# Kernel tuning notes

Measured on AMD Instinct MI355X. Metric: run time of the kernel, lower is better.

The kernel has to match this reference:

```python
import jax, jax.numpy as jnp
import numpy as np

N, E, F, H, O = 50000, 800000, 64, 128, 64
GRID_SIZE, SPLINE_ORDER = 3, 2


def make_grid(in_features, grid_size=GRID_SIZE, spline_order=SPLINE_ORDER, grid_range=(-1.0, 1.0)):
    h = (grid_range[1] - grid_range[0]) / grid_size
    pts = jnp.arange(-spline_order, grid_size + spline_order + 1, dtype=jnp.float32) * h + grid_range[0]
    return jnp.tile(pts[None, :], (in_features, 1))  # [in, grid_size + 2*order + 1]


def b_splines(x, grid, spline_order=SPLINE_ORDER):
    # x: [B, in], grid: [in, G+2k+1] -> bases [B, in, G+k]
    xe = x[..., None]
    bases = ((xe >= grid[:, :-1]) & (xe < grid[:, 1:])).astype(x.dtype)
    for k in range(1, spline_order + 1):
        bases = ((xe - grid[:, : -(k + 1)]) / (grid[:, k:-1] - grid[:, : -(k + 1)]) * bases[..., :-1]
                 + (grid[:, k + 1:] - xe) / (grid[:, k + 1:] - grid[:, 1:-k]) * bases[..., 1:])
    return bases


def setup_inputs() -> dict:
    key = jax.random.key(0)
    ks = jax.random.split(key, 12)
    x = jax.random.normal(ks[0], (N, F), dtype=jnp.float32)
    contexts = jax.random.normal(ks[1], (E, F), dtype=jnp.float32)
    attn = jax.random.uniform(ks[2], (E,), dtype=jnp.float32)
    seg_ids = jnp.sort(jax.random.randint(ks[3], (E,), 0, N, dtype=jnp.int32))
    s = 0.05
    Wn = jax.random.normal(ks[4], (H, F), dtype=jnp.float32) * s
    bn = jnp.zeros((H,), dtype=jnp.float32)
    Wc = jax.random.normal(ks[5], (H, F), dtype=jnp.float32) * s
    bc = jnp.zeros((H,), dtype=jnp.float32)
    Wu = jax.random.normal(ks[6], (O, H), dtype=jnp.float32) * s
    bu = jnp.zeros((O,), dtype=jnp.float32)
    n_coef = GRID_SIZE + SPLINE_ORDER
    base_w = jax.random.normal(ks[7], (O, O), dtype=jnp.float32) * s
    spline_w = jax.random.normal(ks[8], (O, O, n_coef), dtype=jnp.float32) * s
    spline_scaler = jnp.ones((O, O), dtype=jnp.float32)
    grid = make_grid(O)
    return dict(x=x, contexts=contexts, attn=attn, seg_ids=seg_ids, Wn=Wn, bn=bn,
                Wc=Wc, bc=bc, Wu=Wu, bu=bu, base_w=base_w, spline_w=spline_w,
                spline_scaler=spline_scaler, grid=grid)


def reference(x, contexts, attn, seg_ids, Wn, bn, Wc, bc, Wu, bu, base_w, spline_w, spline_scaler, grid):
    n = x.shape[0]
    # per-edge context transform, attention weighting
    ctx_t = contexts @ Wc.T + bc                      # [E, H]
    weighted = ctx_t * attn[:, None]                  # [E, H]
    seg_sum = jax.ops.segment_sum(weighted, seg_ids, num_segments=n)        # [N, H]
    deg = jax.ops.segment_sum(jnp.ones_like(attn), seg_ids, num_segments=n)  # [N]
    ctx_agg = seg_sum / jnp.maximum(deg, 1.0)[:, None]  # mean over edges per node
    x_t = x @ Wn.T + bn                               # [N, H]
    upd = (x_t + ctx_agg) @ Wu.T + bu                 # [N, O]
    # KANLinear (efficient-kan): silu base path + b-spline path
    base_out = jax.nn.silu(upd) @ base_w.T            # [N, O]
    bases = b_splines(upd, grid)                      # [N, O, G+k]
    scaled_sw = spline_w * spline_scaler[..., None]   # [O, O, G+k]
    spline_out = jnp.einsum('bik,oik->bo', bases, scaled_sw)
    kan_out = base_out + spline_out
    # nodes with no contexts keep their raw features (num_features == output_dim)
    return jnp.where(deg[:, None] > 0, kan_out, x)
```

## Files before the change

### kernel.cpp

```cpp
#include <hip/hip_runtime.h>
#include <hip/hip_bf16.h>

#define NN 50000
#define NE 800000

typedef short short8 __attribute__((ext_vector_type(8)));
typedef float f32x4 __attribute__((ext_vector_type(4)));
typedef unsigned short ushort_t;

static __device__ __forceinline__ unsigned bits(float f) { return __float_as_uint(f); }
static __device__ __forceinline__ float hi_f(float v) {
  return __uint_as_float(bits(v) & 0xFFFF0000u);
}
static __device__ __forceinline__ ushort_t hi_u(float v) { return (ushort_t)(bits(v) >> 16); }
static __device__ __forceinline__ unsigned pack_hi(float v0, float v1) {
  return (bits(v0) >> 16) | (bits(v1) & 0xFFFF0000u);
}
static __device__ __forceinline__ unsigned pack_lo(float v0, float v1) {
  float l0 = v0 - hi_f(v0), l1 = v1 - hi_f(v1);
  return (bits(l0) >> 16) | (bits(l1) & 0xFFFF0000u);
}

#define MFMA(a, b, c) __builtin_amdgcn_mfma_f32_16x16x32_bf16(a, b, c, 0, 0, 0)

__global__ __launch_bounds__(256) void kA_pack_off(
    const float* __restrict__ Wn, const float* __restrict__ Wc,
    const float* __restrict__ Wu, const float* __restrict__ base_w,
    const float* __restrict__ spline_w, const float* __restrict__ scaler,
    const int* __restrict__ seg,
    ushort_t* __restrict__ p1h, ushort_t* __restrict__ p2h,
    ushort_t* __restrict__ p3h, int* __restrict__ off) {
  int t = blockIdx.x * 256 + threadIdx.x;
  if (t < 4096) {
    int l = t & 63, lm = l & 15, lk = l >> 4;
    if (t < 2048) {
      int nt = t >> 8, ks = (t >> 6) & 3;
      int h = nt * 16 + lm;
#pragma unroll
      for (int j = 0; j < 8; ++j) {
        int f = ks * 32 + lk * 8 + j;
        float v = (f < 64) ? Wn[h * 64 + f] : Wc[h * 64 + (f - 64)];
        p1h[t * 8 + j] = hi_u(v);
      }
    }
    if (t < 1024) {
      int nt = t >> 8, ks = (t >> 6) & 3;
      int o = nt * 16 + lm;
#pragma unroll
      for (int j = 0; j < 8; ++j) {
        int hh = ks * 32 + lk * 8 + j;
        p2h[t * 8 + j] = hi_u(Wu[o * 128 + hh]);
      }
    }
    if (t < 3072) {
      int nt = t / 768, ks = (t >> 6) % 12;
      int o = nt * 16 + lm;
#pragma unroll
      for (int j = 0; j < 8; ++j) {
        int k = ks * 32 + lk * 8 + j;
        int i = k / 6, c = k % 6;
        float v = (c == 0) ? base_w[o * 64 + i]
                           : spline_w[(o * 64 + i) * 5 + (c - 1)] * scaler[o * 64 + i];
        p3h[t * 8 + j] = hi_u(v);
      }
    }
  }
  int e = t;
  if (e < NE) {
    int s1 = seg[e];
    if (e == 0) {
      for (int n = 0; n <= s1; ++n) off[n] = 0;
    } else {
      int s0 = seg[e - 1];
      for (int n = s0 + 1; n <= s1; ++n) off[n] = e;
    }
    if (e == NE - 1) {
      for (int n = s1 + 1; n <= NN; ++n) off[n] = NE;
    }
  }
}

__global__ __launch_bounds__(256) void k1_edge_agg(
    const float* __restrict__ contexts, const float* __restrict__ attn,
    const int* __restrict__ off, ushort_t* __restrict__ Sph,
    ushort_t* __restrict__ Spl, float* __restrict__ aprime,
    float* __restrict__ degw) {
  int n = blockIdx.x * 4 + (threadIdx.x >> 6);
  int lane = threadIdx.x & 63;
  if (n >= NN) return;
  int s = off[n];
  int e_end = off[n + 1];
  int deg_i = e_end - s;

  int sub = lane >> 4;
  int fq = lane & 15;
  const float4* ctx4 = (const float4*)contexts;

  float4 S = make_float4(0.f, 0.f, 0.f, 0.f);
  float A = 0.f;
  if (deg_i > 0) {
    int last = e_end - 1;
    for (int e0 = s; e0 < e_end; e0 += 16) {
      float a[4];
      float4 c[4];
#pragma unroll
      for (int u = 0; u < 4; ++u) {
        int eu = e0 + 4 * u + sub;
        a[u] = (eu < e_end) ? attn[eu] : 0.f;
        c[u] = ctx4[(size_t)min(eu, last) * 16 + fq];
      }
#pragma unroll
      for (int u = 0; u < 4; ++u) {
        S.x += a[u] * c[u].x;
        S.y += a[u] * c[u].y;
        S.z += a[u] * c[u].z;
        S.w += a[u] * c[u].w;
        A += a[u];
      }
    }
  }
#pragma unroll
  for (int m = 16; m <= 32; m <<= 1) {
    S.x += __shfl_xor(S.x, m);
    S.y += __shfl_xor(S.y, m);
    S.z += __shfl_xor(S.z, m);
    S.w += __shfl_xor(S.w, m);
    A += __shfl_xor(A, m);
  }
  float deg = (float)deg_i;
  float inv = 1.f / fmaxf(deg, 1.f);
  if (lane < 16) {
    float ox = S.x * inv, oy = S.y * inv, oz = S.z * inv, ow = S.w * inv;
    uint2 hp, lp;
    hp.x = pack_hi(ox, oy);
    hp.y = pack_hi(oz, ow);
    lp.x = pack_lo(ox, oy);
    lp.y = pack_lo(oz, ow);
    *(uint2*)&Sph[(size_t)n * 64 + lane * 4] = hp;
    *(uint2*)&Spl[(size_t)n * 64 + lane * 4] = lp;
  }
  if (lane == 0) { aprime[n] = A * inv; degw[n] = deg; }
}

__global__ __launch_bounds__(256, 3) void k234(
    const float* __restrict__ x,
    const ushort_t* __restrict__ Sph, const ushort_t* __restrict__ Spl,
    const float* __restrict__ aprime, const float* __restrict__ degw,
    const float* __restrict__ bn, const float* __restrict__ bc,
    const float* __restrict__ bu,
    const ushort_t* __restrict__ p1h, const ushort_t* __restrict__ p2h,
    const ushort_t* __restrict__ p3h,
    const float* __restrict__ gridp, float* __restrict__ out) {
  __shared__ __align__(16) unsigned char arena[49152];
  __shared__ float ap[64], degl[64];
  ushort_t* Uh = (ushort_t*)arena;
  ushort_t* Ul = (ushort_t*)(arena + 16384);
  ushort_t* Th = (ushort_t*)(arena + 32768);
  ushort_t* Vh = (ushort_t*)arena;

  int tid = threadIdx.x;
  int n0 = blockIdx.x * 64;
  int w = tid >> 6, l = tid & 63;
  int lm = l & 15, lk = l >> 4;
  const short8* P1h = (const short8*)p1h;
  const short8* P2h = (const short8*)p2h;
  const short8* P3h = (const short8*)p3h;

  short8 B1[2][4], B2[4];
#pragma unroll
  for (int q2 = 0; q2 < 2; ++q2)
#pragma unroll
    for (int ks = 0; ks < 4; ++ks) B1[q2][ks] = P1h[((2 * w + q2) * 4 + ks) * 64 + l];
#pragma unroll
  for (int ks = 0; ks < 4; ++ks) B2[ks] = P2h[(w * 4 + ks) * 64 + l];

  float g[8];
#pragma unroll
  for (int j = 0; j < 8; ++j) g[j] = gridp[j];
  float r1[7], r2[6];
#pragma unroll
  for (int j = 0; j < 7; ++j) r1[j] = 1.f / (g[j + 1] - g[j]);
#pragma unroll
  for (int j = 0; j < 6; ++j) r2[j] = 1.f / (g[j + 2] - g[j]);
  float buv = bu[w * 16 + lm];

  {
    const float4* x4 = (const float4*)x;
    const uint4* Sh4 = (const uint4*)Sph;
    const uint4* Sl4 = (const uint4*)Spl;
    for (int q = tid; q < 1024; q += 256) {
      int row = q >> 4, slot = q & 15;
      int n = n0 + row;
      int idx = (row * 128 + slot * 8) ^ ((row & 7) << 3);
      if (slot < 8) {
        float4 a = make_float4(0.f, 0.f, 0.f, 0.f), b = a;
        if (n < NN) {
          a = x4[(size_t)n * 16 + slot * 2];
          b = x4[(size_t)n * 16 + slot * 2 + 1];
        }
        uint4 hp, lp;
        hp.x = pack_hi(a.x, a.y); hp.y = pack_hi(a.z, a.w);
        hp.z = pack_hi(b.x, b.y); hp.w = pack_hi(b.z, b.w);
        lp.x = pack_lo(a.x, a.y); lp.y = pack_lo(a.z, a.w);
        lp.z = pack_lo(b.x, b.y); lp.w = pack_lo(b.z, b.w);
        *(uint4*)&Uh[idx] = hp;
        *(uint4*)&Ul[idx] = lp;
      } else {
        uint4 vh = make_uint4(0u, 0u, 0u, 0u), vl = vh;
        if (n < NN) {
          vh = Sh4[(size_t)n * 8 + (slot & 7)];
          vl = Sl4[(size_t)n * 8 + (slot & 7)];
        }
        *(uint4*)&Uh[idx] = vh;
        *(uint4*)&Ul[idx] = vl;
      }
    }
  }
  if (tid < 64) {
    int n = n0 + tid;
    ap[tid] = (n < NN) ? aprime[n] : 0.f;
    degl[tid] = (n < NN) ? degw[n] : 1.f;
  }
  __syncthreads();

  int swzA = (lm & 7) << 3;

  f32x4 acc1[2][4];
#pragma unroll
  for (int q2 = 0; q2 < 2; ++q2)
#pragma unroll
    for (int mt = 0; mt < 4; ++mt) acc1[q2][mt] = (f32x4){0.f, 0.f, 0.f, 0.f};
#pragma unroll
  for (int ks = 0; ks < 4; ++ks) {
    short8 ah[4], al[4];
#pragma unroll
    for (int mt = 0; mt < 4; ++mt) {
      int ai = ((mt * 16 + lm) * 128 + ks * 32 + lk * 8) ^ swzA;
      ah[mt] = *(const short8*)&Uh[ai];
      al[mt] = *(const short8*)&Ul[ai];
    }
#pragma unroll
    for (int q2 = 0; q2 < 2; ++q2)
#pragma unroll
      for (int mt = 0; mt < 4; ++mt) {
        acc1[q2][mt] = MFMA(ah[mt], B1[q2][ks], acc1[q2][mt]);
        acc1[q2][mt] = MFMA(al[mt], B1[q2][ks], acc1[q2][mt]);
      }
  }
#pragma unroll
  for (int q2 = 0; q2 < 2; ++q2) {
    int h = (2 * w + q2) * 16 + lm;
    float bnv = bn[h], bcv = bc[h];
#pragma unroll
    for (int mt = 0; mt < 4; ++mt) {
#pragma unroll
      for (int r = 0; r < 4; ++r) {
        int node = mt * 16 + lk * 4 + r;
        float t = acc1[q2][mt][r] + bnv + ap[node] * bcv;
        Th[(node * 128 + h) ^ ((node & 7) << 3)] = hi_u(t);
      }
    }
  }
  __syncthreads();

  short8 B3[12];
#pragma unroll
  for (int ks = 0; ks < 12; ++ks) B3[ks] = P3h[(w * 12 + ks) * 64 + l];

  f32x4 acc2[4];
#pragma unroll
  for (int mt = 0; mt < 4; ++mt) acc2[mt] = (f32x4){0.f, 0.f, 0.f, 0.f};
#pragma unroll
  for (int ks = 0; ks < 4; ++ks) {
#pragma unroll
    for (int mt = 0; mt < 4; ++mt) {
      int ai = ((mt * 16 + lm) * 128 + ks * 32 + lk * 8) ^ swzA;
      short8 ah = *(const short8*)&Th[ai];
      acc2[mt] = MFMA(ah, B2[ks], acc2[mt]);
    }
  }

#pragma unroll
  for (int half = 0; half < 2; ++half) {
#pragma unroll
    for (int ms = 0; ms < 2; ++ms) {
      int mt = half * 2 + ms;
#pragma unroll
      for (int r = 0; r < 4; ++r) {
        float xv = acc2[mt][r] + buv;
        float sil = xv / (1.f + __expf(-xv));
        float b0[7], b1[6], b2[5];
#pragma unroll
        for (int q = 0; q < 7; ++q) b0[q] = (xv >= g[q] && xv < g[q + 1]) ? 1.f : 0.f;
#pragma unroll
        for (int q = 0; q < 6; ++q)
          b1[q] = (xv - g[q]) * r1[q] * b0[q] + (g[q + 2] - xv) * r1[q + 1] * b0[q + 1];
#pragma unroll
        for (int q = 0; q < 5; ++q)
          b2[q] = (xv - g[q]) * r2[q] * b1[q] + (g[q + 3] - xv) * r2[q + 1] * b1[q + 1];
        int ln = ms * 16 + lk * 4 + r;
        int base = ln * 392 + (w * 16 + lm) * 6;
        *(unsigned*)&Vh[base + 0] = pack_hi(sil, b2[0]);
        *(unsigned*)&Vh[base + 2] = pack_hi(b2[1], b2[2]);
        *(unsigned*)&Vh[base + 4] = pack_hi(b2[3], b2[4]);
      }
    }
    __syncthreads();

    f32x4 accK[2];
    accK[0] = (f32x4){0.f, 0.f, 0.f, 0.f};
    accK[1] = (f32x4){0.f, 0.f, 0.f, 0.f};
#pragma unroll
    for (int ks = 0; ks < 12; ++ks) {
#pragma unroll
      for (int s = 0; s < 2; ++s) {
        short8 ah = *(const short8*)&Vh[(s * 16 + lm) * 392 + ks * 32 + lk * 8];
        accK[s] = MFMA(ah, B3[ks], accK[s]);
      }
    }
    if (half == 0) __syncthreads();

#pragma unroll
    for (int s = 0; s < 2; ++s) {
      int o = w * 16 + lm;
#pragma unroll
      for (int r = 0; r < 4; ++r) {
        int node = half * 32 + s * 16 + lk * 4 + r;
        int n = n0 + node;
        if (n < NN) {
          float val = accK[s][r];
          if (degl[node] <= 0.f) val = x[(size_t)n * 64 + o];
          out[(size_t)n * 64 + o] = val;
        }
      }
    }
  }
}

extern "C" void kernel_launch(void* const* d_in, const int* in_sizes, int n_in,
                              void* d_out, int out_size, void* d_ws, size_t ws_size,
                              hipStream_t stream) {
  const float* x        = (const float*)d_in[0];
  const float* contexts = (const float*)d_in[1];
  const float* attn     = (const float*)d_in[2];
  const int*   seg      = (const int*)d_in[3];
  const float* Wn       = (const float*)d_in[4];
  const float* bn       = (const float*)d_in[5];
  const float* Wc       = (const float*)d_in[6];
  const float* bc       = (const float*)d_in[7];
  const float* Wu       = (const float*)d_in[8];
  const float* bu       = (const float*)d_in[9];
  const float* base_w   = (const float*)d_in[10];
  const float* spline_w = (const float*)d_in[11];
  const float* scaler   = (const float*)d_in[12];
  const float* gridp    = (const float*)d_in[13];
  float* out = (float*)d_out;

  ushort_t* us  = (ushort_t*)d_ws;
  ushort_t* Sph = us;
  ushort_t* Spl = Sph + 3200000;
  ushort_t* p1h = Spl + 3200000;
  ushort_t* p2h = p1h + 16384;
  ushort_t* p3h = p2h + 8192;
  float* aprime = (float*)(p3h + 24576);
  float* degw   = aprime + 50000;
  int*   off    = (int*)(degw + 50000);

  kA_pack_off<<<3125, 256, 0, stream>>>(Wn, Wc, Wu, base_w, spline_w, scaler, seg,
                                        p1h, p2h, p3h, off);
  k1_edge_agg<<<12500, 256, 0, stream>>>(contexts, attn, off, Sph, Spl, aprime, degw);
  k234<<<782, 256, 0, stream>>>(x, Sph, Spl, aprime, degw, bn, bc, bu,
                                p1h, p2h, p3h, gridp, out);
}
```

Measured before the change: 73.15 us.

## Fuse edge aggregation into node MLP/KAN kernel with 512-thread blocks

Merges the per-node edge aggregation kernel into the dense node kernel, so each 64-node block first reduces its own edges straight into shared memory instead of writing and reading back split-bf16 aggregates, attn means and degrees through global memory. Blocks grow to 8 waves, split 2x4 over node and output tiles, and each wave aggregates 8 nodes serially. This removes one launch and the intermediate global traffic. In exchange only 782 blocks carry the whole edge gather, and the irregular, latency-bound gather now runs serially per wave in the same kernel as the MFMA stages, which may lower latency hiding.

```diff
diff --git a/kernel.cpp b/kernel.cpp
--- a/kernel.cpp
+++ b/kernel.cpp
@@ -80,72 +80,10 @@
   }
 }
 
-__global__ __launch_bounds__(256) void k1_edge_agg(
+__global__ __launch_bounds__(512, 4) void k1234(
+    const float* __restrict__ x,
     const float* __restrict__ contexts, const float* __restrict__ attn,
-    const int* __restrict__ off, ushort_t* __restrict__ Sph,
-    ushort_t* __restrict__ Spl, float* __restrict__ aprime,
-    float* __restrict__ degw) {
-  int n = blockIdx.x * 4 + (threadIdx.x >> 6);
-  int lane = threadIdx.x & 63;
-  if (n >= NN) return;
-  int s = off[n];
-  int e_end = off[n + 1];
-  int deg_i = e_end - s;
-
-  int sub = lane >> 4;
-  int fq = lane & 15;
-  const float4* ctx4 = (const float4*)contexts;
-
-  float4 S = make_float4(0.f, 0.f, 0.f, 0.f);
-  float A = 0.f;
-  if (deg_i > 0) {
-    int last = e_end - 1;
-    for (int e0 = s; e0 < e_end; e0 += 16) {
-      float a[4];
-      float4 c[4];
-#pragma unroll
-      for (int u = 0; u < 4; ++u) {
-        int eu = e0 + 4 * u + sub;
-        a[u] = (eu < e_end) ? attn[eu] : 0.f;
-        c[u] = ctx4[(size_t)min(eu, last) * 16 + fq];
-      }
-#pragma unroll
-      for (int u = 0; u < 4; ++u) {
-        S.x += a[u] * c[u].x;
-        S.y += a[u] * c[u].y;
-        S.z += a[u] * c[u].z;
-        S.w += a[u] * c[u].w;
-        A += a[u];
-      }
-    }
-  }
-#pragma unroll
-  for (int m = 16; m <= 32; m <<= 1) {
-    S.x += __shfl_xor(S.x, m);
-    S.y += __shfl_xor(S.y, m);
-    S.z += __shfl_xor(S.z, m);
-    S.w += __shfl_xor(S.w, m);
-    A += __shfl_xor(A, m);
-  }
-  float deg = (float)deg_i;
-  float inv = 1.f / fmaxf(deg, 1.f);
-  if (lane < 16) {
-    float ox = S.x * inv, oy = S.y * inv, oz = S.z * inv, ow = S.w * inv;
-    uint2 hp, lp;
-    hp.x = pack_hi(ox, oy);
-    hp.y = pack_hi(oz, ow);
-    lp.x = pack_lo(ox, oy);
-    lp.y = pack_lo(oz, ow);
-    *(uint2*)&Sph[(size_t)n * 64 + lane * 4] = hp;
-    *(uint2*)&Spl[(size_t)n * 64 + lane * 4] = lp;
-  }
-  if (lane == 0) { aprime[n] = A * inv; degw[n] = deg; }
-}
-
-__global__ __launch_bounds__(256, 3) void k234(
-    const float* __restrict__ x,
-    const ushort_t* __restrict__ Sph, const ushort_t* __restrict__ Spl,
-    const float* __restrict__ aprime, const float* __restrict__ degw,
+    const int* __restrict__ off,
     const float* __restrict__ bn, const float* __restrict__ bc,
     const float* __restrict__ bu,
     const ushort_t* __restrict__ p1h, const ushort_t* __restrict__ p2h,
@@ -161,19 +99,144 @@
   int tid = threadIdx.x;
   int n0 = blockIdx.x * 64;
   int w = tid >> 6, l = tid & 63;
+  int wm = w >> 2, wn = w & 3;
   int lm = l & 15, lk = l >> 4;
   const short8* P1h = (const short8*)p1h;
   const short8* P2h = (const short8*)p2h;
   const short8* P3h = (const short8*)p3h;
 
+  {
+    const float4* x4 = (const float4*)x;
+    int row = tid >> 3, slot = tid & 7;
+    int n = n0 + row;
+    float4 a = make_float4(0.f, 0.f, 0.f, 0.f), b = a;
+    if (n < NN) {
+      a = x4[(size_t)n * 16 + slot * 2];
+      b = x4[(size_t)n * 16 + slot * 2 + 1];
+    }
+    uint4 hp, lp;
+    hp.x = pack_hi(a.x, a.y); hp.y = pack_hi(a.z, a.w);
+    hp.z = pack_hi(b.x, b.y); hp.w = pack_hi(b.z, b.w);
+    lp.x = pack_lo(a.x, a.y); lp.y = pack_lo(a.z, a.w);
+    lp.z = pack_lo(b.x, b.y); lp.w = pack_lo(b.z, b.w);
+    int idx = (row * 128 + slot * 8) ^ ((row & 7) << 3);
+    *(uint4*)&Uh[idx] = hp;
+    *(uint4*)&Ul[idx] = lp;
+  }
+
+  {
+    int nb = n0 + w * 8;
+    int offv = 0;
+    if (l < 9) offv = off[min(nb + l, NN)];
+    int sub = l >> 4, fq = l & 15;
+    const float4* ctx4 = (const float4*)contexts;
+#pragma unroll 1
+    for (int i = 0; i < 8; ++i) {
+      int s = __shfl(offv, i);
+      int e_end = __shfl(offv, i + 1);
+      int deg_i = e_end - s;
+      float4 S = make_float4(0.f, 0.f, 0.f, 0.f);
+      float A = 0.f;
+      if (deg_i > 0) {
+        int last = e_end - 1;
+        for (int e0 = s; e0 < e_end; e0 += 16) {
+          float a[4];
+          float4 c[4];
+#pragma unroll
+          for (int u = 0; u < 4; ++u) {
+            int eu = e0 + 4 * u + sub;
+            a[u] = (eu < e_end) ? attn[eu] : 0.f;
+            c[u] = ctx4[(size_t)min(eu, last) * 16 + fq];
+          }
+#pragma unroll
+          for (int u = 0; u < 4; ++u) {
+            S.x += a[u] * c[u].x;
+            S.y += a[u] * c[u].y;
+            S.z += a[u] * c[u].z;
+            S.w += a[u] * c[u].w;
+            A += a[u];
+          }
+        }
+      }
+#pragma unroll
+      for (int m = 16; m <= 32; m <<= 1) {
+        S.x += __shfl_xor(S.x, m);
+        S.y += __shfl_xor(S.y, m);
+        S.z += __shfl_xor(S.z, m);
+        S.w += __shfl_xor(S.w, m);
+        A += __shfl_xor(A, m);
+      }
+      float deg = (float)deg_i;
+      float inv = 1.f / fmaxf(deg, 1.f);
+      int row = w * 8 + i;
+      if (l < 16) {
+        float ox = S.x * inv, oy = S.y * inv, oz = S.z * inv, ow = S.w * inv;
+        uint2 hp, lp;
+        hp.x = pack_hi(ox, oy);
+        hp.y = pack_hi(oz, ow);
+        lp.x = pack_lo(ox, oy);
+        lp.y = pack_lo(oz, ow);
+        int idx = (row * 128 + 64 + l * 4) ^ ((row & 7) << 3);
+        *(uint2*)&Uh[idx] = hp;
+        *(uint2*)&Ul[idx] = lp;
+      }
+      if (l == 0) { ap[row] = A * inv; degl[row] = deg; }
+    }
+  }
+
   short8 B1[2][4], B2[4];
 #pragma unroll
-  for (int q2 = 0; q2 < 2; ++q2)
-#pragma unroll
-    for (int ks = 0; ks < 4; ++ks) B1[q2][ks] = P1h[((2 * w + q2) * 4 + ks) * 64 + l];
-#pragma unroll
-  for (int ks = 0; ks < 4; ++ks) B2[ks] = P2h[(w * 4 + ks) * 64 + l];
-
+  for (int q = 0; q < 2; ++q)
+#pragma unroll
+    for (int ks = 0; ks < 4; ++ks) B1[q][ks] = P1h[((2 * wn + q) * 4 + ks) * 64 + l];
+#pragma unroll
+  for (int ks = 0; ks < 4; ++ks) B2[ks] = P2h[(wn * 4 + ks) * 64 + l];
+
+  __syncthreads();
+
+  int swzA = (lm & 7) << 3;
+
+  f32x4 acc1[2][2];
+#pragma unroll
+  for (int q = 0; q < 2; ++q)
+#pragma unroll
+    for (int ms = 0; ms < 2; ++ms) acc1[q][ms] = (f32x4){0.f, 0.f, 0.f, 0.f};
+#pragma unroll
+  for (int ks = 0; ks < 4; ++ks) {
+    short8 ah[2], al[2];
+#pragma unroll
+    for (int ms = 0; ms < 2; ++ms) {
+      int ai = (((2 * wm + ms) * 16 + lm) * 128 + ks * 32 + lk * 8) ^ swzA;
+      ah[ms] = *(const short8*)&Uh[ai];
+      al[ms] = *(const short8*)&Ul[ai];
+    }
+#pragma unroll
+    for (int q = 0; q < 2; ++q)
+#pragma unroll
+      for (int ms = 0; ms < 2; ++ms) {
+        acc1[q][ms] = MFMA(ah[ms], B1[q][ks], acc1[q][ms]);
+        acc1[q][ms] = MFMA(al[ms], B1[q][ks], acc1[q][ms]);
+      }
+  }
+#pragma unroll
+  for (int q = 0; q < 2; ++q) {
+    int h = (2 * wn + q) * 16 + lm;
+    float bnv = bn[h], bcv = bc[h];
+#pragma unroll
+    for (int ms = 0; ms < 2; ++ms) {
+#pragma unroll
+      for (int r = 0; r < 4; ++r) {
+        int node = (2 * wm + ms) * 16 + lk * 4 + r;
+        float t = acc1[q][ms][r] + bnv + ap[node] * bcv;
+        Th[(node * 128 + h) ^ ((node & 7) << 3)] = hi_u(t);
+      }
+    }
+  }
+  __syncthreads();
+
+  short8 B3[12];
+#pragma unroll
+  for (int ks = 0; ks < 12; ++ks) B3[ks] = P3h[(wn * 12 + ks) * 64 + l];
   float g[8];
 #pragma unroll
   for (int j = 0; j < 8; ++j) g[j] = gridp[j];
@@ -182,156 +245,66 @@
   for (int j = 0; j < 7; ++j) r1[j] = 1.f / (g[j + 1] - g[j]);
 #pragma unroll
   for (int j = 0; j < 6; ++j) r2[j] = 1.f / (g[j + 2] - g[j]);
-  float buv = bu[w * 16 + lm];
-
-  {
-    const float4* x4 = (const float4*)x;
-    const uint4* Sh4 = (const uint4*)Sph;
-    const uint4* Sl4 = (const uint4*)Spl;
-    for (int q = tid; q < 1024; q += 256) {
-      int row = q >> 4, slot = q & 15;
-      int n = n0 + row;
-      int idx = (row * 128 + slot * 8) ^ ((row & 7) << 3);
-      if (slot < 8) {
-        float4 a = make_float4(0.f, 0.f, 0.f, 0.f), b = a;
-        if (n < NN) {
-          a = x4[(size_t)n * 16 + slot * 2];
-          b = x4[(size_t)n * 16 + slot * 2 + 1];
+  float buv = bu[wn * 16 + lm];
+
+  f32x4 acc2[2];
+  acc2[0] = (f32x4){0.f, 0.f, 0.f, 0.f};
+  acc2[1] = (f32x4){0.f, 0.f, 0.f, 0.f};
+#pragma unroll
+  for (int ks = 0; ks < 4; ++ks) {
+#pragma unroll
+    for (int ms = 0; ms < 2; ++ms) {
+      int ai = (((2 * wm + ms) * 16 + lm) * 128 + ks * 32 + lk * 8) ^ swzA;
+      short8 ah = *(const short8*)&Th[ai];
+      acc2[ms] = MFMA(ah, B2[ks], acc2[ms]);
+    }
+  }
+
+#pragma unroll
+  for (int half = 0; half < 2; ++half) {
+    if (wm == half) {
+#pragma unroll
+      for (int ms = 0; ms < 2; ++ms) {
+#pragma unroll
+        for (int r = 0; r < 4; ++r) {
+          float xv = acc2[ms][r] + buv;
+          float sil = xv / (1.f + __expf(-xv));
+          float b0[7], b1[6], b2[5];
+#pragma unroll
+          for (int q = 0; q < 7; ++q) b0[q] = (xv >= g[q] && xv < g[q + 1]) ? 1.f : 0.f;
+#pragma unroll
+          for (int q = 0; q < 6; ++q)
+            b1[q] = (xv - g[q]) * r1[q] * b0[q] + (g[q + 2] - xv) * r1[q + 1] * b0[q + 1];
+#pragma unroll
+          for (int q = 0; q < 5; ++q)
+            b2[q] = (xv - g[q]) * r2[q] * b1[q] + (g[q + 3] - xv) * r2[q + 1] * b1[q + 1];
+          int ln = ms * 16 + lk * 4 + r;
+          int base = ln * 392 + (wn * 16 + lm) * 6;
+          *(unsigned*)&Vh[base + 0] = pack_hi(sil, b2[0]);
+          *(unsigned*)&Vh[base + 2] = pack_hi(b2[1], b2[2]);
+          *(unsigned*)&Vh[base + 4] = pack_hi(b2[3], b2[4]);
         }
-        uint4 hp, lp;
-        hp.x = pack_hi(a.x, a.y); hp.y = pack_hi(a.z, a.w);
-        hp.z = pack_hi(b.x, b.y); hp.w = pack_hi(b.z, b.w);
-        lp.x = pack_lo(a.x, a.y); lp.y = pack_lo(a.z, a.w);
-        lp.z = pack_lo(b.x, b.y); lp.w = pack_lo(b.z, b.w);
-        *(uint4*)&Uh[idx] = hp;
-        *(uint4*)&Ul[idx] = lp;
-      } else {
-        uint4 vh = make_uint4(0u, 0u, 0u, 0u), vl = vh;
-        if (n < NN) {
-          vh = Sh4[(size_t)n * 8 + (slot & 7)];
-          vl = Sl4[(size_t)n * 8 + (slot & 7)];
-        }
-        *(uint4*)&Uh[idx] = vh;
-        *(uint4*)&Ul[idx] = vl;
-      }
-    }
-  }
-  if (tid < 64) {
-    int n = n0 + tid;
-    ap[tid] = (n < NN) ? aprime[n] : 0.f;
-    degl[tid] = (n < NN) ? degw[n] : 1.f;
-  }
-  __syncthreads();
-
-  int swzA = (lm & 7) << 3;
-
-  f32x4 acc1[2][4];
-#pragma unroll
-  for (int q2 = 0; q2 < 2; ++q2)
-#pragma unroll
-    for (int mt = 0; mt < 4; ++mt) acc1[q2][mt] = (f32x4){0.f, 0.f, 0.f, 0.f};
-#pragma unroll
-  for (int ks = 0; ks < 4; ++ks) {
-    short8 ah[4], al[4];
-#pragma unroll
-    for (int mt = 0; mt < 4; ++mt) {
-      int ai = ((mt * 16 + lm) * 128 + ks * 32 + lk * 8) ^ swzA;
-      ah[mt] = *(const short8*)&Uh[ai];
-      al[mt] = *(const short8*)&Ul[ai];
-    }
-#pragma unroll
-    for (int q2 = 0; q2 < 2; ++q2)
-#pragma unroll
-      for (int mt = 0; mt < 4; ++mt) {
-        acc1[q2][mt] = MFMA(ah[mt], B1[q2][ks], acc1[q2][mt]);
-        acc1[q2][mt] = MFMA(al[mt], B1[q2][ks], acc1[q2][mt]);
-      }
-  }
-#pragma unroll
-  for (int q2 = 0; q2 < 2; ++q2) {
-    int h = (2 * w + q2) * 16 + lm;
-    float bnv = bn[h], bcv = bc[h];
-#pragma unroll
-    for (int mt = 0; mt < 4; ++mt) {
-#pragma unroll
-      for (int r = 0; r < 4; ++r) {
-        int node = mt * 16 + lk * 4 + r;
-        float t = acc1[q2][mt][r] + bnv + ap[node] * bcv;
-        Th[(node * 128 + h) ^ ((node & 7) << 3)] = hi_u(t);
-      }
-    }
-  }
-  __syncthreads();
-
-  short8 B3[12];
-#pragma unroll
-  for (int ks = 0; ks < 12; ++ks) B3[ks] = P3h[(w * 12 + ks) * 64 + l];
-
-  f32x4 acc2[4];
-#pragma unroll
-  for (int mt = 0; mt < 4; ++mt) acc2[mt] = (f32x4){0.f, 0.f, 0.f, 0.f};
-#pragma unroll
-  for (int ks = 0; ks < 4; ++ks) {
-#pragma unroll
-    for (int mt = 0; mt < 4; ++mt) {
-      int ai = ((mt * 16 + lm) * 128 + ks * 32 + lk * 8) ^ swzA;
-      short8 ah = *(const short8*)&Th[ai];
-      acc2[mt] = MFMA(ah, B2[ks], acc2[mt]);
-    }
-  }
-
-#pragma unroll
-  for (int half = 0; half < 2; ++half) {
-#pragma unroll
-    for (int ms = 0; ms < 2; ++ms) {
-      int mt = half * 2 + ms;
-#pragma unroll
-      for (int r = 0; r < 4; ++r) {
-        float xv = acc2[mt][r] + buv;
-        float sil = xv / (1.f + __expf(-xv));
-        float b0[7], b1[6], b2[5];
-#pragma unroll
-        for (int q = 0; q < 7; ++q) b0[q] = (xv >= g[q] && xv < g[q + 1]) ? 1.f : 0.f;
-#pragma unroll
-        for (int q = 0; q < 6; ++q)
-          b1[q] = (xv - g[q]) * r1[q] * b0[q] + (g[q + 2] - xv) * r1[q + 1] * b0[q + 1];
-#pragma unroll
-        for (int q = 0; q < 5; ++q)
-          b2[q] = (xv - g[q]) * r2[q] * b1[q] + (g[q + 3] - xv) * r2[q + 1] * b1[q + 1];
-        int ln = ms * 16 + lk * 4 + r;
-        int base = ln * 392 + (w * 16 + lm) * 6;
-        *(unsigned*)&Vh[base + 0] = pack_hi(sil, b2[0]);
-        *(unsigned*)&Vh[base + 2] = pack_hi(b2[1], b2[2]);
-        *(unsigned*)&Vh[base + 4] = pack_hi(b2[3], b2[4]);
       }
     }
     __syncthreads();
 
-    f32x4 accK[2];
-    accK[0] = (f32x4){0.f, 0.f, 0.f, 0.f};
-    accK[1] = (f32x4){0.f, 0.f, 0.f, 0.f};
+    f32x4 accK = (f32x4){0.f, 0.f, 0.f, 0.f};
 #pragma unroll
     for (int ks = 0; ks < 12; ++ks) {
-#pragma unroll
-      for (int s = 0; s < 2; ++s) {
-        short8 ah = *(const short8*)&Vh[(s * 16 + lm) * 392 + ks * 32 + lk * 8];
-        accK[s] = MFMA(ah, B3[ks], accK[s]);
-      }
+      short8 ah = *(const short8*)&Vh[(wm * 16 + lm) * 392 + ks * 32 + lk * 8];
+      accK = MFMA(ah, B3[ks], accK);
     }
     if (half == 0) __syncthreads();
 
-#pragma unroll
-    for (int s = 0; s < 2; ++s) {
-      int o = w * 16 + lm;
-#pragma unroll
-      for (int r = 0; r < 4; ++r) {
-        int node = half * 32 + s * 16 + lk * 4 + r;
-        int n = n0 + node;
-        if (n < NN) {
-          float val = accK[s][r];
-          if (degl[node] <= 0.f) val = x[(size_t)n * 64 + o];
-          out[(size_t)n * 64 + o] = val;
-        }
+    int o = wn * 16 + lm;
+#pragma unroll
+    for (int r = 0; r < 4; ++r) {
+      int node = half * 32 + wm * 16 + lk * 4 + r;
+      int n = n0 + node;
+      if (n < NN) {
+        float val = accK[r];
+        if (degl[node] <= 0.f) val = x[(size_t)n * 64 + o];
+        out[(size_t)n * 64 + o] = val;
       }
     }
   }
@@ -357,18 +330,13 @@
   float* out = (float*)d_out;
 
   ushort_t* us  = (ushort_t*)d_ws;
-  ushort_t* Sph = us;
-  ushort_t* Spl = Sph + 3200000;
-  ushort_t* p1h = Spl + 3200000;
+  ushort_t* p1h = us;
   ushort_t* p2h = p1h + 16384;
   ushort_t* p3h = p2h + 8192;
-  float* aprime = (float*)(p3h + 24576);
-  float* degw   = aprime + 50000;
-  int*   off    = (int*)(degw + 50000);
+  int*   off    = (int*)(p3h + 24576);
 
   kA_pack_off<<<3125, 256, 0, stream>>>(Wn, Wc, Wu, base_w, spline_w, scaler, seg,
                                         p1h, p2h, p3h, off);
-  k1_edge_agg<<<12500, 256, 0, stream>>>(contexts, attn, off, Sph, Spl, aprime, degw);
-  k234<<<782, 256, 0, stream>>>(x, Sph, Spl, aprime, degw, bn, bc, bu,
-                                p1h, p2h, p3h, gridp, out);
-}
+  k1234<<<782, 512, 0, stream>>>(x, contexts, attn, off, bn, bc, bu,
+                                 p1h, p2h, p3h, gridp, out);
+}
```

Measured after the change: 67.49 us. 1.08x faster.

## Shrink LDS arena and stream weight fragments to raise k234 occupancy

Applied to the files above, without the earlier changes.

Reuses the Ul LDS buffer for the intermediate T tile instead of a separate third region, cutting the shared arena from 48KB to 32KB. Weight fragments B1 and B3 are now loaded from global or cache inside the MFMA loops rather than held in registers for the whole kernel, and the grid and bias setup moves later, which lowers register pressure. Launch bounds go from 3 to 4 blocks per SM so more waves can be resident and hide latency. The cost is two extra barriers and repeated global loads of the weight fragments inside the loops.

```diff
diff --git a/kernel.cpp b/kernel.cpp
--- a/kernel.cpp
+++ b/kernel.cpp
@@ -142,7 +142,7 @@
   if (lane == 0) { aprime[n] = A * inv; degw[n] = deg; }
 }
 
-__global__ __launch_bounds__(256, 3) void k234(
+__global__ __launch_bounds__(256, 4) void k234(
     const float* __restrict__ x,
     const ushort_t* __restrict__ Sph, const ushort_t* __restrict__ Spl,
     const float* __restrict__ aprime, const float* __restrict__ degw,
@@ -151,11 +151,10 @@
     const ushort_t* __restrict__ p1h, const ushort_t* __restrict__ p2h,
     const ushort_t* __restrict__ p3h,
     const float* __restrict__ gridp, float* __restrict__ out) {
-  __shared__ __align__(16) unsigned char arena[49152];
+  __shared__ __align__(16) unsigned char arena[32768];
   __shared__ float ap[64], degl[64];
   ushort_t* Uh = (ushort_t*)arena;
   ushort_t* Ul = (ushort_t*)(arena + 16384);
-  ushort_t* Th = (ushort_t*)(arena + 32768);
   ushort_t* Vh = (ushort_t*)arena;
 
   int tid = threadIdx.x;
@@ -166,23 +165,9 @@
   const short8* P2h = (const short8*)p2h;
   const short8* P3h = (const short8*)p3h;
 
-  short8 B1[2][4], B2[4];
-#pragma unroll
-  for (int q2 = 0; q2 < 2; ++q2)
-#pragma unroll
-    for (int ks = 0; ks < 4; ++ks) B1[q2][ks] = P1h[((2 * w + q2) * 4 + ks) * 64 + l];
+  short8 B2[4];
 #pragma unroll
   for (int ks = 0; ks < 4; ++ks) B2[ks] = P2h[(w * 4 + ks) * 64 + l];
-
-  float g[8];
-#pragma unroll
-  for (int j = 0; j < 8; ++j) g[j] = gridp[j];
-  float r1[7], r2[6];
-#pragma unroll
-  for (int j = 0; j < 7; ++j) r1[j] = 1.f / (g[j + 1] - g[j]);
-#pragma unroll
-  for (int j = 0; j < 6; ++j) r2[j] = 1.f / (g[j + 2] - g[j]);
-  float buv = bu[w * 16 + lm];
 
   {
     const float4* x4 = (const float4*)x;
@@ -227,45 +212,41 @@
 
   f32x4 acc1[2][4];
 #pragma unroll
-  for (int q2 = 0; q2 < 2; ++q2)
-#pragma unroll
-    for (int mt = 0; mt < 4; ++mt) acc1[q2][mt] = (f32x4){0.f, 0.f, 0.f, 0.f};
+  for (int q = 0; q < 2; ++q)
+#pragma unroll
+    for (int mt = 0; mt < 4; ++mt) acc1[q][mt] = (f32x4){0.f, 0.f, 0.f, 0.f};
 #pragma unroll
   for (int ks = 0; ks < 4; ++ks) {
-    short8 ah[4], al[4];
+    short8 bh0 = P1h[((2 * w + 0) * 4 + ks) * 64 + l];
+    short8 bh1 = P1h[((2 * w + 1) * 4 + ks) * 64 + l];
 #pragma unroll
     for (int mt = 0; mt < 4; ++mt) {
       int ai = ((mt * 16 + lm) * 128 + ks * 32 + lk * 8) ^ swzA;
-      ah[mt] = *(const short8*)&Uh[ai];
-      al[mt] = *(const short8*)&Ul[ai];
-    }
-#pragma unroll
-    for (int q2 = 0; q2 < 2; ++q2)
-#pragma unroll
-      for (int mt = 0; mt < 4; ++mt) {
-        acc1[q2][mt] = MFMA(ah[mt], B1[q2][ks], acc1[q2][mt]);
-        acc1[q2][mt] = MFMA(al[mt], B1[q2][ks], acc1[q2][mt]);
-      }
-  }
-#pragma unroll
-  for (int q2 = 0; q2 < 2; ++q2) {
-    int h = (2 * w + q2) * 16 + lm;
+      short8 ah = *(const short8*)&Uh[ai];
+      short8 al = *(const short8*)&Ul[ai];
+      acc1[0][mt] = MFMA(ah, bh0, acc1[0][mt]);
+      acc1[0][mt] = MFMA(al, bh0, acc1[0][mt]);
+      acc1[1][mt] = MFMA(ah, bh1, acc1[1][mt]);
+      acc1[1][mt] = MFMA(al, bh1, acc1[1][mt]);
+    }
+  }
+  __syncthreads();
+
+#pragma unroll
+  for (int q = 0; q < 2; ++q) {
+    int h = (2 * w + q) * 16 + lm;
     float bnv = bn[h], bcv = bc[h];
 #pragma unroll
     for (int mt = 0; mt < 4; ++mt) {
 #pragma unroll
       for (int r = 0; r < 4; ++r) {
         int node = mt * 16 + lk * 4 + r;
-        float t = acc1[q2][mt][r] + bnv + ap[node] * bcv;
-        Th[(node * 128 + h) ^ ((node & 7) << 3)] = hi_u(t);
+        float t = acc1[q][mt][r] + bnv + ap[node] * bcv;
+        Ul[(node * 128 + h) ^ ((node & 7) << 3)] = hi_u(t);
       }
     }
   }
   __syncthreads();
-
-  short8 B3[12];
-#pragma unroll
-  for (int ks = 0; ks < 12; ++ks) B3[ks] = P3h[(w * 12 + ks) * 64 + l];
 
   f32x4 acc2[4];
 #pragma unroll
@@ -275,10 +256,21 @@
 #pragma unroll
     for (int mt = 0; mt < 4; ++mt) {
       int ai = ((mt * 16 + lm) * 128 + ks * 32 + lk * 8) ^ swzA;
-      short8 ah = *(const short8*)&Th[ai];
+      short8 ah = *(const short8*)&Ul[ai];
       acc2[mt] = MFMA(ah, B2[ks], acc2[mt]);
     }
   }
+  __syncthreads();
+
+  float g[8];
+#pragma unroll
+  for (int j = 0; j < 8; ++j) g[j] = gridp[j];
+  float r1[7], r2[6];
+#pragma unroll
+  for (int j = 0; j < 7; ++j) r1[j] = 1.f / (g[j + 1] - g[j]);
+#pragma unroll
+  for (int j = 0; j < 6; ++j) r2[j] = 1.f / (g[j + 2] - g[j]);
+  float buv = bu[w * 16 + lm];
 
 #pragma unroll
   for (int half = 0; half < 2; ++half) {
@@ -312,13 +304,14 @@
     accK[1] = (f32x4){0.f, 0.f, 0.f, 0.f};
 #pragma unroll
     for (int ks = 0; ks < 12; ++ks) {
+      short8 bh = P3h[(w * 12 + ks) * 64 + l];
 #pragma unroll
       for (int s = 0; s < 2; ++s) {
         short8 ah = *(const short8*)&Vh[(s * 16 + lm) * 392 + ks * 32 + lk * 8];
-        accK[s] = MFMA(ah, B3[ks], accK[s]);
-      }
-    }
-    if (half == 0) __syncthreads();
+        accK[s] = MFMA(ah, bh, accK[s]);
+      }
+    }
+    __syncthreads();
 
 #pragma unroll
     for (int s = 0; s < 2; ++s) {
```

Result: faster. 70.73 us (-3.3%).
